# Optimization experiments

Measured on AMD Instinct MI355X. Metric: run time of the kernel, lower is better.

## Reference

```python
import jax, jax.numpy as jnp
import numpy as np

B, N, D = 2, 8192, 1024
H, Dh = 16, 64
P = H * Dh
EPS = 1e-6
DECAY_BIAS_SHIFT = 2.0


def setup_inputs() -> dict:
    key = jax.random.key(0)
    ks = jax.random.split(key, 7)
    s_in = 1.0 / np.sqrt(D)
    s_out = 1.0 / np.sqrt(P)
    return {
        "x": jax.random.normal(ks[0], (B, N, D), jnp.float32),
        "Wq": jax.random.normal(ks[1], (D, P), jnp.float32) * s_in,
        "Wk": jax.random.normal(ks[2], (D, P), jnp.float32) * s_in,
        "Wv": jax.random.normal(ks[3], (D, P), jnp.float32) * s_in,
        "Wo": jax.random.normal(ks[4], (P, D), jnp.float32) * s_out,
        "Wa": jax.random.normal(ks[5], (D, H), jnp.float32) * s_in,
        "ba": jnp.zeros((H,), jnp.float32),
    }


def _elu_plus_one(x):
    return jax.nn.elu(x) + 1.0


def _ssd_scan(q, k, v, a, eps):
    # q,k,v: (B,H,N,Dh); a: (B,H,N) in (0,1)
    # Recurrence: S_t = a_t*S_{t-1} + k_t v_t^T ; z_t = a_t*z_{t-1} + k_t
    # out_t = (q_t @ S_t) / (q_t . z_t + eps)
    qT = jnp.moveaxis(q, 2, 0)  # (N,B,H,Dh)
    kT = jnp.moveaxis(k, 2, 0)
    vT = jnp.moveaxis(v, 2, 0)
    aT = jnp.moveaxis(a, 2, 0)  # (N,B,H)

    Bb, Hh, _, Dk = q.shape
    Dv = v.shape[-1]
    S0 = jnp.zeros((Bb, Hh, Dk, Dv), q.dtype)
    z0 = jnp.zeros((Bb, Hh, Dk), q.dtype)

    def step(carry, inp):
        S, z = carry
        qt, kt, vt, at = inp
        S = at[..., None, None] * S + kt[..., :, None] * vt[..., None, :]
        z = at[..., None] * z + kt
        num = jnp.einsum("bhk,bhkv->bhv", qt, S)
        den = jnp.einsum("bhk,bhk->bh", qt, z) + eps
        return (S, z), num / den[..., None]

    _, outT = jax.lax.scan(step, (S0, z0), (qT, kT, vT, aT))
    return jnp.moveaxis(outT, 0, 2)  # (B,H,N,Dv)


def reference(x, Wq, Wk, Wv, Wo, Wa, ba):
    b, n, _ = x.shape
    q = (x @ Wq).reshape(b, n, H, Dh).transpose(0, 2, 1, 3)
    k = (x @ Wk).reshape(b, n, H, Dh).transpose(0, 2, 1, 3)
    v = (x @ Wv).reshape(b, n, H, Dh).transpose(0, 2, 1, 3)
    q = _elu_plus_one(q)
    k = _elu_plus_one(k)
    a = jax.nn.sigmoid(x @ Wa + ba + DECAY_BIAS_SHIFT)  # (B,N,H)
    a = a.transpose(0, 2, 1)  # (B,H,N)
    out = _ssd_scan(q, k, v, a, EPS)  # (B,H,N,Dh)
    out = out.transpose(0, 2, 1, 3).reshape(b, n, P)
    return out @ Wo
```

## Files before the change

kernel.cpp:

```cpp
#include <hip/hip_runtime.h>
#include <stdint.h>

#define HH 16
#define DH 64
#define DD 1024
#define PP 1024
#define NNLEN 8192
#define BBATCH 2
#define MM (BBATCH*NNLEN)
#define CCHUNK 128
#define LCH 64
#define NGRP 16
#define GCH 8
#define EPSV 1e-6f

typedef unsigned short u16;
typedef __attribute__((ext_vector_type(4))) unsigned short u16x4;
typedef __attribute__((ext_vector_type(8))) unsigned short u16x8;
typedef __attribute__((ext_vector_type(8))) __bf16 bf16x8;
typedef __attribute__((ext_vector_type(4))) float f32x4;

__device__ __forceinline__ u16 f2bf(float f) {
  unsigned x = __float_as_uint(f);
  return (u16)((x + 0x7fffu + ((x >> 16) & 1u)) >> 16);
}
__device__ __forceinline__ float bf2f(u16 u) {
  return __uint_as_float(((unsigned)u) << 16);
}

__device__ __forceinline__ void gl2lds16(const void* g, void* l) {
  __builtin_amdgcn_global_load_lds(
      reinterpret_cast<__attribute__((address_space(1))) void*>(
          reinterpret_cast<uintptr_t>(g)),
      reinterpret_cast<__attribute__((address_space(3))) void*>(
          reinterpret_cast<uintptr_t>(l)),
      16, 0, 0);
}

__device__ __forceinline__ bf16x8 ldsw(const u16* base, int row, int col) {
  union { u16x8 u; bf16x8 b; } cv;
  cv.u = *(const u16x8*)&base[row * 64 + (col ^ ((row & 7) << 3))];
  return cv.b;
}

__global__ __launch_bounds__(256)
void convert_x(const float* __restrict__ in, u16* __restrict__ out) {
  size_t i = ((size_t)blockIdx.x * 256 + threadIdx.x) * 8;
  f32x4 a = *(const f32x4*)(in + i);
  f32x4 b = *(const f32x4*)(in + i + 4);
  u16x8 o;
  o[0] = f2bf(a[0]); o[1] = f2bf(a[1]); o[2] = f2bf(a[2]); o[3] = f2bf(a[3]);
  o[4] = f2bf(b[0]); o[5] = f2bf(b[1]); o[6] = f2bf(b[2]); o[7] = f2bf(b[3]);
  *(u16x8*)(out + i) = o;
}

__global__ __launch_bounds__(256)
void wa_prep(const float* __restrict__ Wa, u16* __restrict__ WaT) {
  int idx = blockIdx.x * 256 + threadIdx.x;
  WaT[idx] = f2bf(Wa[(idx & 1023) * 16 + (idx >> 10)]);
}

__global__ __launch_bounds__(256)
void transpose_f32_bf16(const float* __restrict__ in, u16* __restrict__ out) {
  __shared__ float tile[32][33];
  int bx = blockIdx.x * 32, by = blockIdx.y * 32;
  int tx = threadIdx.x & 31, ty = threadIdx.x >> 5;
  for (int i = ty; i < 32; i += 8)
    tile[i][tx] = in[(size_t)(by + i) * 1024 + bx + tx];
  __syncthreads();
  for (int i = ty; i < 32; i += 8)
    out[(size_t)(bx + i) * 1024 + by + tx] = f2bf(tile[tx][i]);
}

__global__ __launch_bounds__(256)
void a_proj(const u16* __restrict__ xb, const u16* __restrict__ WaT,
            const float* __restrict__ ba, float* __restrict__ abuf) {
  __shared__ __align__(16) u16 As[256 * 32];
  __shared__ __align__(16) u16 Bs[16 * 32];
  const int tid = threadIdx.x;
  const int brow = blockIdx.x * 256;
  const int l = tid & 63, wid = tid >> 6;
  const int la = l & 15, kb8 = (l >> 4) * 8;
  const int sr = tid >> 2, se = (tid & 3) * 8;

  f32x4 acc[4];
#pragma unroll
  for (int mi = 0; mi < 4; ++mi) acc[mi] = (f32x4){0.f, 0.f, 0.f, 0.f};

  for (int kt = 0; kt < 32; ++kt) {
    const int k0 = kt * 32;
    __syncthreads();
#pragma unroll
    for (int i = 0; i < 4; ++i)
      gl2lds16(xb + (size_t)(brow + i * 64 + sr) * DD + k0 + se,
               &As[i * 2048 + wid * 512]);
    if (wid == 0)
      gl2lds16(WaT + (size_t)(l >> 2) * DD + k0 + (l & 3) * 8, &Bs[0]);
    __syncthreads();
    union { u16x8 u; bf16x8 b; } cvb;
    cvb.u = *(const u16x8*)&Bs[la * 32 + kb8];
#pragma unroll
    for (int mi = 0; mi < 4; ++mi) {
      union { u16x8 u; bf16x8 b; } cva;
      cva.u = *(const u16x8*)&As[(wid * 64 + mi * 16 + la) * 32 + kb8];
      acc[mi] = __builtin_amdgcn_mfma_f32_16x16x32_bf16(cva.b, cvb.b, acc[mi], 0, 0, 0);
    }
  }
  const float bav = ba[la];
#pragma unroll
  for (int mi = 0; mi < 4; ++mi)
#pragma unroll
    for (int rr = 0; rr < 4; ++rr) {
      int row = brow + wid * 64 + mi * 16 + ((l >> 4) << 2) + rr;
      float t = acc[mi][rr] + bav + 2.0f;
      abuf[(size_t)row * HH + la] = 1.f / (1.f + __expf(-t));
    }
}

template<int NCT, int ROUTE>
__global__ __launch_bounds__(512)
void gemm8p(const u16* __restrict__ A, const u16* __restrict__ Bt,
            void* __restrict__ Cout) {
  __shared__ __align__(16) u16 As[2][256 * 64];
  __shared__ __align__(16) u16 Bs[2][256 * 64];
  const int tid = threadIdx.x;
  const int nwg = gridDim.x;
  const int f = blockIdx.x;
  const int swz = (f & 7) * (nwg >> 3) + (f >> 3);
  const int brow = (swz / NCT) * 256;
  const int bcol = (swz % NCT) * 256;
  const int l = tid & 63;
  const int wid = tid >> 6;
  const int wr = wid >> 2;
  const int wc = wid & 3;
  const int la = l & 15, kb8 = (l >> 4) * 8;
  const int K = 1024;
  const int srow = l >> 3;
  const int scol = ((l & 7) * 8) ^ (srow << 3);
  const int ldso = (wid * 2) * 512;

  f32x4 acc[8][4];
#pragma unroll
  for (int i = 0; i < 8; ++i)
#pragma unroll
    for (int j = 0; j < 4; ++j) acc[i][j] = (f32x4){0.f, 0.f, 0.f, 0.f};

#pragma unroll
  for (int h = 0; h < 2; ++h)
#pragma unroll
    for (int j = 0; j < 2; ++j) {
      const int r0 = h * 128 + (wid * 2 + j) * 8 + srow;
      gl2lds16(A  + (size_t)(brow + r0) * K + scol, &As[0][h * 8192 + ldso + j * 512]);
      gl2lds16(Bt + (size_t)(bcol + r0) * K + scol, &Bs[0][h * 8192 + ldso + j * 512]);
    }
  asm volatile("s_waitcnt vmcnt(0)" ::: "memory");
  __builtin_amdgcn_s_barrier();

  const int NKT = K / 64;
  for (int kt = 0; kt < NKT; ++kt) {
    const u16* lA = As[kt & 1];
    const u16* lB = Bs[kt & 1];
    u16* nA = As[(kt + 1) & 1];
    u16* nB = Bs[(kt + 1) & 1];
    const int knext = (kt + 1) * 64;
    const bool more = (kt + 1 < NKT);

    bf16x8 af[4][2], bfr[2][2];
#pragma unroll
    for (int p = 0; p < 4; ++p) {
      const int miH = (p >> 1);
      const int niH = (p == 1 || p == 2) ? 1 : 0;
      const bool doA = (p == 0 || p == 2);
      const bool doB = (p != 2);
      if (doA) {
#pragma unroll
        for (int m2 = 0; m2 < 4; ++m2)
#pragma unroll
          for (int kk = 0; kk < 2; ++kk)
            af[m2][kk] = ldsw(lA, wr * 128 + miH * 64 + m2 * 16 + la, kk * 32 + kb8);
      }
      if (doB) {
#pragma unroll
        for (int n2 = 0; n2 < 2; ++n2)
#pragma unroll
          for (int kk = 0; kk < 2; ++kk)
            bfr[n2][kk] = ldsw(lB, wc * 64 + niH * 32 + n2 * 16 + la, kk * 32 + kb8);
      }
      if (more && p == 0) {
#pragma unroll
        for (int h = 0; h < 2; ++h)
#pragma unroll
          for (int j = 0; j < 2; ++j) {
            const int r0 = h * 128 + (wid * 2 + j) * 8 + srow;
            gl2lds16(A + (size_t)(brow + r0) * K + knext + scol,
                     nA + h * 8192 + ldso + j * 512);
          }
      }
      if (more && p == 1) {
#pragma unroll
        for (int h = 0; h < 2; ++h)
#pragma unroll
          for (int j = 0; j < 2; ++j) {
            const int r0 = h * 128 + (wid * 2 + j) * 8 + srow;
            gl2lds16(Bt + (size_t)(bcol + r0) * K + knext + scol,
                     nB + h * 8192 + ldso + j * 512);
          }
      }
      __builtin_amdgcn_s_barrier();
      __builtin_amdgcn_s_setprio(1);
#pragma unroll
      for (int m2 = 0; m2 < 4; ++m2)
#pragma unroll
        for (int n2 = 0; n2 < 2; ++n2)
#pragma unroll
          for (int kk = 0; kk < 2; ++kk)
            acc[miH * 4 + m2][niH * 2 + n2] = __builtin_amdgcn_mfma_f32_16x16x32_bf16(
                af[m2][kk], bfr[n2][kk], acc[miH * 4 + m2][niH * 2 + n2], 0, 0, 0);
      __builtin_amdgcn_s_setprio(0);
      if (p == 3) asm volatile("s_waitcnt vmcnt(0)" ::: "memory");
      __builtin_amdgcn_s_barrier();
    }
  }

  const int wrow = wr * 128, wcol = wc * 64;
  if (ROUTE) {
    u16* base = (u16*)Cout + (size_t)(bcol >> 10) * ((size_t)MM * 1024);
    const bool act = (bcol < 2048);
#pragma unroll
    for (int mi = 0; mi < 8; ++mi)
#pragma unroll
      for (int ni = 0; ni < 4; ++ni)
#pragma unroll
        for (int rr = 0; rr < 4; ++rr) {
          int row = brow + wrow + mi * 16 + ((l >> 4) << 2) + rr;
          int c2 = (bcol & 1023) + wcol + ni * 16 + la;
          float v = acc[mi][ni][rr];
          if (act) v = v > 0.f ? v + 1.f : __expf(v);
          base[(size_t)row * 1024 + c2] = f2bf(v);
        }
  } else {
#pragma unroll
    for (int mi = 0; mi < 8; ++mi)
#pragma unroll
      for (int ni = 0; ni < 4; ++ni)
#pragma unroll
        for (int rr = 0; rr < 4; ++rr) {
          int row = brow + wrow + mi * 16 + ((l >> 4) << 2) + rr;
          int col = bcol + wcol + ni * 16 + la;
          ((float*)Cout)[(size_t)row * 1024 + col] = acc[mi][ni][rr];
        }
  }
}

__global__ __launch_bounds__(256)
void chunk_local(const u16* __restrict__ kb, const u16* __restrict__ vb,
                 const float* __restrict__ abuf,
                 u16* __restrict__ Sbuf, float* __restrict__ zbuf,
                 float* __restrict__ cAbuf) {
  const int blk = blockIdx.x;
  const int c = blk & (CCHUNK - 1);
  const int h = (blk >> 7) & (HH - 1);
  const int b = blk >> 11;
  const int rowbase = b * NNLEN + c * LCH;
  __shared__ __align__(16) u16 KT[64 * 64];
  __shared__ __align__(16) u16 VTl[64 * 64];
  __shared__ float wsh[64];
  const int tid = threadIdx.x;
  const int r = tid >> 2, e = (tid & 3) * 16;

  const u16* kp = kb + (size_t)(rowbase + r) * PP + h * DH + e;
  const u16* vp = vb + (size_t)(rowbase + r) * PP + h * DH + e;
  u16x8 k0 = *(const u16x8*)kp, k1 = *(const u16x8*)(kp + 8);
  u16x8 v0 = *(const u16x8*)vp, v1 = *(const u16x8*)(vp + 8);

  if (tid < 64) {
    float v = __logf(abuf[(size_t)(rowbase + tid) * HH + h]);
#pragma unroll
    for (int d = 1; d < 64; d <<= 1) {
      float u = __shfl_up(v, d);
      if (tid >= d) v += u;
    }
    cAbuf[(size_t)blk * 64 + tid] = v;
    float tot = __shfl(v, 63);
    wsh[tid] = __expf(tot - v);
  }
  __syncthreads();

  {
    const float wt = wsh[r];
#pragma unroll
    for (int j = 0; j < 8; ++j) {
      int d0 = e + j, d1 = e + 8 + j;
      KT[d0 * 64 + (r ^ ((d0 & 7) << 3))] = f2bf(bf2f(k0[j]) * wt);
      KT[d1 * 64 + (r ^ ((d1 & 7) << 3))] = f2bf(bf2f(k1[j]) * wt);
      VTl[d0 * 64 + (r ^ ((d0 & 7) << 3))] = v0[j];
      VTl[d1 * 64 + (r ^ ((d1 & 7) << 3))] = v1[j];
    }
  }
  __syncthreads();

  const int l = tid & 63, w = tid >> 6;
  const int kb8 = (l >> 4) << 3, la = l & 15;
  f32x4 s[4];
#pragma unroll
  for (int ni = 0; ni < 4; ++ni) s[ni] = (f32x4){0.f, 0.f, 0.f, 0.f};
#pragma unroll
  for (int kk = 0; kk < 2; ++kk) {
    bf16x8 av = ldsw(VTl, 16 * w + la, kk * 32 + kb8);
#pragma unroll
    for (int ni = 0; ni < 4; ++ni)
      s[ni] = __builtin_amdgcn_mfma_f32_16x16x32_bf16(
          av, ldsw(KT, 16 * ni + la, kk * 32 + kb8), s[ni], 0, 0, 0);
  }
  u16* Sc = Sbuf + (size_t)blk * 4096;
  const int dw = 16 * w + ((l >> 4) << 2);
#pragma unroll
  for (int ni = 0; ni < 4; ++ni)
#pragma unroll
    for (int rr = 0; rr < 4; ++rr)
      Sc[(dw + rr) * 64 + 16 * ni + la] = f2bf(s[ni][rr]);

  {
    const int dk = tid >> 2, tq = (tid & 3) * 16, swk = (dk & 7) << 3;
    float zp = 0.f;
#pragma unroll
    for (int i = 0; i < 16; ++i) zp += bf2f(KT[dk * 64 + ((tq + i) ^ swk)]);
    zp += __shfl_xor(zp, 1);
    zp += __shfl_xor(zp, 2);
    if ((tid & 3) == 0) zbuf[(size_t)blk * 64 + dk] = zp;
  }
}

__global__ __launch_bounds__(256)
void scan_group(u16* __restrict__ Sbuf, float* __restrict__ zbuf,
                const float* __restrict__ cAbuf,
                float* __restrict__ GAgg, float* __restrict__ zGAgg,
                float* __restrict__ dpbuf) {
  const int j = blockIdx.x & 3;
  const int g = (blockIdx.x >> 2) & (NGRP - 1);
  const int bh = blockIdx.x >> 6;
  const int c0 = g * GCH;
  const size_t cb = (size_t)bh * CCHUNK;
  const int elem = j * 1024 + threadIdx.x * 4;

  float dch[GCH];
#pragma unroll
  for (int i = 0; i < GCH; ++i)
    dch[i] = __expf(cAbuf[(cb + c0 + i) * 64 + 63]);
  if (j == 0 && threadIdx.x == 0) {
    float rp = 1.f;
#pragma unroll
    for (int i = 0; i < GCH; ++i) { dpbuf[cb + c0 + i] = rp; rp *= dch[i]; }
  }

  f32x4 run = (f32x4){0.f, 0.f, 0.f, 0.f};
  u16x4 cur = *(const u16x4*)&Sbuf[(cb + c0) * 4096 + elem];
#pragma unroll
  for (int i = 0; i < GCH; ++i) {
    u16x4 nxt;
    if (i + 1 < GCH) nxt = *(const u16x4*)&Sbuf[(cb + c0 + i + 1) * 4096 + elem];
    u16x4 o;
#pragma unroll
    for (int jj = 0; jj < 4; ++jj) o[jj] = f2bf(run[jj]);
    *(u16x4*)&Sbuf[(cb + c0 + i) * 4096 + elem] = o;
#pragma unroll
    for (int jj = 0; jj < 4; ++jj) run[jj] = dch[i] * run[jj] + bf2f(cur[jj]);
    cur = nxt;
  }
  *(f32x4*)&GAgg[((size_t)bh * NGRP + g) * 4096 + elem] = run;

  if (j == 0 && threadIdx.x < 64) {
    const int t = threadIdx.x;
    float zr = 0.f;
#pragma unroll
    for (int i = 0; i < GCH; ++i) {
      float curz = zbuf[(cb + c0 + i) * 64 + t];
      zbuf[(cb + c0 + i) * 64 + t] = zr;
      zr = dch[i] * zr + curz;
    }
    zGAgg[((size_t)bh * NGRP + g) * 64 + t] = zr;
  }
}

__global__ __launch_bounds__(1024)
void scan_top(float* __restrict__ GAgg, float* __restrict__ zGAgg,
              const float* __restrict__ cAbuf) {
  const int bh = blockIdx.x;
  const size_t cb = (size_t)bh * CCHUNK;
  __shared__ float Dsh[NGRP];
  if (threadIdx.x < NGRP) {
    float s = 0.f;
#pragma unroll
    for (int i = 0; i < GCH; ++i)
      s += cAbuf[(cb + threadIdx.x * GCH + i) * 64 + 63];
    Dsh[threadIdx.x] = __expf(s);
  }
  __syncthreads();
  const int elem = threadIdx.x * 4;
  float* base = GAgg + (size_t)bh * NGRP * 4096;
  f32x4 run = (f32x4){0.f, 0.f, 0.f, 0.f};
  f32x4 cur = *(const f32x4*)&base[elem];
#pragma unroll
  for (int gg = 0; gg < NGRP; ++gg) {
    f32x4 nxt;
    if (gg + 1 < NGRP) nxt = *(const f32x4*)&base[(gg + 1) * 4096 + elem];
    *(f32x4*)&base[gg * 4096 + elem] = run;
    const float D = Dsh[gg];
#pragma unroll
    for (int jj = 0; jj < 4; ++jj) run[jj] = D * run[jj] + cur[jj];
    cur = nxt;
  }
  if (threadIdx.x < 64) {
    float* zb = zGAgg + (size_t)bh * NGRP * 64;
    float zr = 0.f;
#pragma unroll
    for (int gg = 0; gg < NGRP; ++gg) {
      float a = zb[gg * 64 + threadIdx.x];
      zb[gg * 64 + threadIdx.x] = zr;
      zr = Dsh[gg] * zr + a;
    }
  }
}

__global__ __launch_bounds__(256)
void chunk_out(u16* __restrict__ qb, const u16* __restrict__ kb,
               const u16* __restrict__ vb, const u16* __restrict__ Sbuf,
               const float* __restrict__ zbuf, const float* __restrict__ cAbuf,
               const float* __restrict__ GAgg, const float* __restrict__ zGAgg,
               const float* __restrict__ dpbuf) {
  const int blk = blockIdx.x;
  const int c = blk & (CCHUNK - 1);
  const int h = (blk >> 7) & (HH - 1);
  const int b = blk >> 11;
  const int bh = blk >> 7;
  const int g = c >> 3;
  const int rowbase = b * NNLEN + c * LCH;

  __shared__ __align__(16) u16 Qs[64 * 64];
  __shared__ __align__(16) u16 Ke[64 * 64];
  __shared__ __align__(16) u16 VT[64 * 64];
  __shared__ __align__(16) u16 STs[64 * 64];
  __shared__ __align__(16) u16 Pb[64 * 64];
  __shared__ float cAsh[64], zsh[64], denP[64], qzs[64];

  const int tid = threadIdx.x;
  const int r = tid >> 2, e = (tid & 3) * 16;
  const float dp = dpbuf[blk];

  const u16* qp = qb + (size_t)(rowbase + r) * PP + h * DH + e;
  const u16* kp = kb + (size_t)(rowbase + r) * PP + h * DH + e;
  const u16* vp = vb + (size_t)(rowbase + r) * PP + h * DH + e;
  u16x8 q0 = *(const u16x8*)qp, q1 = *(const u16x8*)(qp + 8);
  u16x8 k0 = *(const u16x8*)kp, k1 = *(const u16x8*)(kp + 8);
  u16x8 v0 = *(const u16x8*)vp, v1 = *(const u16x8*)(vp + 8);
  const u16* sp = Sbuf + (size_t)blk * 4096 + r * 64 + e;
  u16x8 p0 = *(const u16x8*)sp, p1 = *(const u16x8*)(sp + 8);
  const float* gp = GAgg + ((size_t)bh * NGRP + g) * 4096 + r * 64 + e;
  f32x4 g0 = *(const f32x4*)gp, g1 = *(const f32x4*)(gp + 4),
        g2 = *(const f32x4*)(gp + 8), g3 = *(const f32x4*)(gp + 12);
  if (tid < 64) {
    cAsh[tid] = cAbuf[(size_t)blk * 64 + tid];
    zsh[tid] = zbuf[(size_t)blk * 64 + tid]
             + dp * zGAgg[((size_t)bh * NGRP + g) * 64 + tid];
  }
  __syncthreads();

  {
    const float c0c = cAsh[31];
    const int sw = (r & 7) << 3;
    const float qsc = __expf(cAsh[r] - c0c);
    const float ksc = __expf(c0c - cAsh[r]);
    const float ssc = __expf(c0c);
    u16x8 t0, t1, u0, u1, w0, w1;
#pragma unroll
    for (int j = 0; j < 8; ++j) {
      t0[j] = f2bf(bf2f(q0[j]) * qsc);
      t1[j] = f2bf(bf2f(q1[j]) * qsc);
      u0[j] = f2bf(bf2f(k0[j]) * ksc);
      u1[j] = f2bf(bf2f(k1[j]) * ksc);
    }
#pragma unroll
    for (int j = 0; j < 4; ++j) {
      w0[j]     = f2bf((bf2f(p0[j])     + dp * g0[j]) * ssc);
      w0[4 + j] = f2bf((bf2f(p0[4 + j]) + dp * g1[j]) * ssc);
      w1[j]     = f2bf((bf2f(p1[j])     + dp * g2[j]) * ssc);
      w1[4 + j] = f2bf((bf2f(p1[4 + j]) + dp * g3[j]) * ssc);
    }
    *(u16x8*)&Qs[r * 64 + (e ^ sw)] = t0;
    *(u16x8*)&Qs[r * 64 + ((e + 8) ^ sw)] = t1;
    *(u16x8*)&Ke[r * 64 + (e ^ sw)] = u0;
    *(u16x8*)&Ke[r * 64 + ((e + 8) ^ sw)] = u1;
    *(u16x8*)&STs[r * 64 + (e ^ sw)] = w0;
    *(u16x8*)&STs[r * 64 + ((e + 8) ^ sw)] = w1;
#pragma unroll
    for (int j = 0; j < 8; ++j) {
      int d0 = e + j, d1 = e + 8 + j;
      VT[d0 * 64 + (r ^ ((d0 & 7) << 3))] = v0[j];
      VT[d1 * 64 + (r ^ ((d1 & 7) << 3))] = v1[j];
    }
    if (tid < 64) zsh[tid] *= ssc;
  }
  __syncthreads();

  const int l = tid & 63, w = tid >> 6;
  const int kb8 = (l >> 4) << 3, la = l & 15;

  bf16x8 aq[2];
  f32x4 p[4];
#pragma unroll
  for (int ni = 0; ni < 4; ++ni) p[ni] = (f32x4){0.f, 0.f, 0.f, 0.f};
#pragma unroll
  for (int kk = 0; kk < 2; ++kk) {
    aq[kk] = ldsw(Qs, 16 * w + la, kk * 32 + kb8);
#pragma unroll
    for (int ni = 0; ni < 4; ++ni)
      p[ni] = __builtin_amdgcn_mfma_f32_16x16x32_bf16(
          aq[kk], ldsw(Ke, 16 * ni + la, kk * 32 + kb8), p[ni], 0, 0, 0);
  }

  const int tw = 16 * w + ((l >> 4) << 2);
  float rsum[4] = {0.f, 0.f, 0.f, 0.f};
#pragma unroll
  for (int ni = 0; ni < 4; ++ni)
#pragma unroll
    for (int rr = 0; rr < 4; ++rr) {
      int s = 16 * ni + la, t = tw + rr;
      float v = (s <= t) ? p[ni][rr] : 0.f;
      p[ni][rr] = v;
      rsum[rr] += v;
    }
#pragma unroll
  for (int d = 1; d < 16; d <<= 1)
#pragma unroll
    for (int rr = 0; rr < 4; ++rr) rsum[rr] += __shfl_xor(rsum[rr], d);
  if (la == 0)
#pragma unroll
    for (int rr = 0; rr < 4; ++rr) denP[tw + rr] = rsum[rr];

#pragma unroll
  for (int ni = 0; ni < 4; ++ni)
#pragma unroll
    for (int rr = 0; rr < 4; ++rr) {
      int t = tw + rr, s = 16 * ni + la;
      Pb[t * 64 + (s ^ ((t & 7) << 3))] = f2bf(p[ni][rr]);
    }

  {
    const int tq = tid >> 2, dq = (tid & 3) * 16, swq = (tq & 7) << 3;
    float qzp = 0.f;
#pragma unroll
    for (int i = 0; i < 16; ++i)
      qzp += bf2f(Qs[tq * 64 + ((dq + i) ^ swq)]) * zsh[dq + i];
    qzp += __shfl_xor(qzp, 1);
    qzp += __shfl_xor(qzp, 2);
    if ((tid & 3) == 0) qzs[tq] = qzp;
  }
  __syncthreads();

  f32x4 o[4];
#pragma unroll
  for (int ni = 0; ni < 4; ++ni) o[ni] = (f32x4){0.f, 0.f, 0.f, 0.f};
#pragma unroll
  for (int kk = 0; kk < 2; ++kk) {
    bf16x8 ap = ldsw(Pb, 16 * w + la, kk * 32 + kb8);
#pragma unroll
    for (int ni = 0; ni < 4; ++ni)
      o[ni] = __builtin_amdgcn_mfma_f32_16x16x32_bf16(
          ap, ldsw(VT, 16 * ni + la, kk * 32 + kb8), o[ni], 0, 0, 0);
  }
#pragma unroll
  for (int kk = 0; kk < 2; ++kk)
#pragma unroll
    for (int ni = 0; ni < 4; ++ni)
      o[ni] = __builtin_amdgcn_mfma_f32_16x16x32_bf16(
          aq[kk], ldsw(STs, 16 * ni + la, kk * 32 + kb8), o[ni], 0, 0, 0);

  float dn[4];
#pragma unroll
  for (int rr = 0; rr < 4; ++rr) dn[rr] = qzs[tw + rr] + denP[tw + rr] + EPSV;
#pragma unroll
  for (int ni = 0; ni < 4; ++ni)
#pragma unroll
    for (int rr = 0; rr < 4; ++rr) {
      int t = tw + rr, dv = 16 * ni + la;
      qb[(size_t)(rowbase + t) * PP + h * DH + dv] = f2bf(o[ni][rr] / dn[rr]);
    }
}

extern "C" void kernel_launch(void* const* d_in, const int* in_sizes, int n_in,
                              void* d_out, int out_size, void* d_ws, size_t ws_size,
                              hipStream_t stream) {
  const float* x  = (const float*)d_in[0];
  const float* Wq = (const float*)d_in[1];
  const float* Wk = (const float*)d_in[2];
  const float* Wv = (const float*)d_in[3];
  const float* Wo = (const float*)d_in[4];
  const float* Wa = (const float*)d_in[5];
  const float* ba = (const float*)d_in[6];

  char* ws = (char*)d_ws;
  size_t off = 0;
  auto carve = [&](size_t bytes) {
    void* p = ws + off;
    off += (bytes + 255) & ~(size_t)255;
    return p;
  };
  u16* xb   = (u16*)carve((size_t)MM * DD * 2);
  u16* WqT  = (u16*)carve((size_t)PP * DD * 2);
  u16* WkT  = (u16*)carve((size_t)PP * DD * 2);
  u16* WvT  = (u16*)carve((size_t)PP * DD * 2);
  u16* WoT  = (u16*)carve((size_t)DD * PP * 2);
  u16* WaT  = (u16*)carve((size_t)HH * DD * 2);
  u16* qb   = (u16*)carve((size_t)MM * PP * 2);
  u16* kb   = (u16*)carve((size_t)MM * PP * 2);
  u16* vb   = (u16*)carve((size_t)MM * PP * 2);
  float* abuf  = (float*)carve((size_t)MM * HH * 4);
  u16*  Sbuf   = (u16*)carve((size_t)BBATCH * HH * CCHUNK * 4096 * 2);
  float* zbuf  = (float*)carve((size_t)BBATCH * HH * CCHUNK * 64 * 4);
  float* cAbuf = (float*)carve((size_t)BBATCH * HH * CCHUNK * 64 * 4);
  float* GAgg  = (float*)carve((size_t)BBATCH * HH * NGRP * 4096 * 4);
  float* zGAgg = (float*)carve((size_t)BBATCH * HH * NGRP * 64 * 4);
  float* dpbuf = (float*)carve((size_t)BBATCH * HH * CCHUNK * 4);

  transpose_f32_bf16<<<dim3(32, 32), 256, 0, stream>>>(Wq, WqT);
  transpose_f32_bf16<<<dim3(32, 32), 256, 0, stream>>>(Wk, WkT);
  transpose_f32_bf16<<<dim3(32, 32), 256, 0, stream>>>(Wv, WvT);
  transpose_f32_bf16<<<dim3(32, 32), 256, 0, stream>>>(Wo, WoT);
  wa_prep<<<64, 256, 0, stream>>>(Wa, WaT);
  convert_x<<<MM * DD / 8 / 256, 256, 0, stream>>>(x, xb);
  a_proj<<<MM / 256, 256, 0, stream>>>(xb, WaT, ba, abuf);

  gemm8p<12, 1><<<(MM / 256) * 12, 512, 0, stream>>>(xb, WqT, qb);

  chunk_local<<<BBATCH * HH * CCHUNK, 256, 0, stream>>>(kb, vb, abuf, Sbuf, zbuf, cAbuf);
  scan_group<<<BBATCH * HH * NGRP * 4, 256, 0, stream>>>(Sbuf, zbuf, cAbuf, GAgg, zGAgg, dpbuf);
  scan_top<<<BBATCH * HH, 1024, 0, stream>>>(GAgg, zGAgg, cAbuf);
  chunk_out<<<BBATCH * HH * CCHUNK, 256, 0, stream>>>(qb, kb, vb, Sbuf, zbuf, cAbuf,
                                                      GAgg, zGAgg, dpbuf);

  gemm8p<4, 0><<<(MM / 256) * 4, 512, 0, stream>>>(qb, WoT, (float*)d_out);
}
```

Before: 285.0 us.

## Fuse chunk-local state with group scan and simplify GEMM k-loop pipeline

Merges the chunk_local and scan_group kernels into one kernel, chunk_local_scan, where each block walks the 8 chunks of a group in sequence and carries the running state in registers. This avoids writing raw chunk states to Sbuf and then reading them back. The GEMM inner loop changes from four barrier-separated phases to two MFMA halves, with one combined prefetch and one barrier per k-step. Grid parallelism for the local state computation drops by a factor of 8, which risks lower occupancy. The GEMM now has less interleaving between loads and compute.

Result: faster. 272.5 us (-4.4%).

```diff
diff --git a/kernel.cpp b/kernel.cpp
--- a/kernel.cpp
+++ b/kernel.cpp
@@ -119,8 +119,8 @@
 
 template<int NCT, int ROUTE>
 __global__ __launch_bounds__(512)
-void gemm8p(const u16* __restrict__ A, const u16* __restrict__ Bt,
-            void* __restrict__ Cout) {
+void gemm_db(const u16* __restrict__ A, const u16* __restrict__ Bt,
+             void* __restrict__ Cout) {
   __shared__ __align__(16) u16 As[2][256 * 64];
   __shared__ __align__(16) u16 Bs[2][256 * 64];
   const int tid = threadIdx.x;
@@ -165,59 +165,61 @@
     const int knext = (kt + 1) * 64;
     const bool more = (kt + 1 < NKT);
 
-    bf16x8 af[4][2], bfr[2][2];
-#pragma unroll
-    for (int p = 0; p < 4; ++p) {
-      const int miH = (p >> 1);
-      const int niH = (p == 1 || p == 2) ? 1 : 0;
-      const bool doA = (p == 0 || p == 2);
-      const bool doB = (p != 2);
-      if (doA) {
-#pragma unroll
-        for (int m2 = 0; m2 < 4; ++m2)
-#pragma unroll
-          for (int kk = 0; kk < 2; ++kk)
-            af[m2][kk] = ldsw(lA, wr * 128 + miH * 64 + m2 * 16 + la, kk * 32 + kb8);
-      }
-      if (doB) {
-#pragma unroll
-        for (int n2 = 0; n2 < 2; ++n2)
-#pragma unroll
-          for (int kk = 0; kk < 2; ++kk)
-            bfr[n2][kk] = ldsw(lB, wc * 64 + niH * 32 + n2 * 16 + la, kk * 32 + kb8);
-      }
-      if (more && p == 0) {
-#pragma unroll
-        for (int h = 0; h < 2; ++h)
-#pragma unroll
-          for (int j = 0; j < 2; ++j) {
-            const int r0 = h * 128 + (wid * 2 + j) * 8 + srow;
-            gl2lds16(A + (size_t)(brow + r0) * K + knext + scol,
-                     nA + h * 8192 + ldso + j * 512);
-          }
-      }
-      if (more && p == 1) {
-#pragma unroll
-        for (int h = 0; h < 2; ++h)
-#pragma unroll
-          for (int j = 0; j < 2; ++j) {
-            const int r0 = h * 128 + (wid * 2 + j) * 8 + srow;
-            gl2lds16(Bt + (size_t)(bcol + r0) * K + knext + scol,
-                     nB + h * 8192 + ldso + j * 512);
-          }
-      }
-      __builtin_amdgcn_s_barrier();
-      __builtin_amdgcn_s_setprio(1);
-#pragma unroll
-      for (int m2 = 0; m2 < 4; ++m2)
-#pragma unroll
-        for (int n2 = 0; n2 < 2; ++n2)
-#pragma unroll
-          for (int kk = 0; kk < 2; ++kk)
-            acc[miH * 4 + m2][niH * 2 + n2] = __builtin_amdgcn_mfma_f32_16x16x32_bf16(
-                af[m2][kk], bfr[n2][kk], acc[miH * 4 + m2][niH * 2 + n2], 0, 0, 0);
-      __builtin_amdgcn_s_setprio(0);
-      if (p == 3) asm volatile("s_waitcnt vmcnt(0)" ::: "memory");
+    bf16x8 af[4][2], bfr[4][2];
+#pragma unroll
+    for (int m2 = 0; m2 < 4; ++m2)
+#pragma unroll
+      for (int kk = 0; kk < 2; ++kk)
+        af[m2][kk] = ldsw(lA, wr * 128 + m2 * 16 + la, kk * 32 + kb8);
+#pragma unroll
+    for (int n2 = 0; n2 < 4; ++n2)
+#pragma unroll
+      for (int kk = 0; kk < 2; ++kk)
+        bfr[n2][kk] = ldsw(lB, wc * 64 + n2 * 16 + la, kk * 32 + kb8);
+
+    __builtin_amdgcn_s_setprio(1);
+#pragma unroll
+    for (int m2 = 0; m2 < 4; ++m2)
+#pragma unroll
+      for (int n2 = 0; n2 < 4; ++n2)
+#pragma unroll
+        for (int kk = 0; kk < 2; ++kk)
+          acc[m2][n2] = __builtin_amdgcn_mfma_f32_16x16x32_bf16(
+              af[m2][kk], bfr[n2][kk], acc[m2][n2], 0, 0, 0);
+    __builtin_amdgcn_s_setprio(0);
+
+#pragma unroll
+    for (int m2 = 0; m2 < 4; ++m2)
+#pragma unroll
+      for (int kk = 0; kk < 2; ++kk)
+        af[m2][kk] = ldsw(lA, wr * 128 + 64 + m2 * 16 + la, kk * 32 + kb8);
+
+    if (more) {
+#pragma unroll
+      for (int h = 0; h < 2; ++h)
+#pragma unroll
+        for (int j = 0; j < 2; ++j) {
+          const int r0 = h * 128 + (wid * 2 + j) * 8 + srow;
+          gl2lds16(A  + (size_t)(brow + r0) * K + knext + scol,
+                   nA + h * 8192 + ldso + j * 512);
+          gl2lds16(Bt + (size_t)(bcol + r0) * K + knext + scol,
+                   nB + h * 8192 + ldso + j * 512);
+        }
+    }
+
+    __builtin_amdgcn_s_setprio(1);
+#pragma unroll
+    for (int m2 = 0; m2 < 4; ++m2)
+#pragma unroll
+      for (int n2 = 0; n2 < 4; ++n2)
+#pragma unroll
+        for (int kk = 0; kk < 2; ++kk)
+          acc[4 + m2][n2] = __builtin_amdgcn_mfma_f32_16x16x32_bf16(
+              af[m2][kk], bfr[n2][kk], acc[4 + m2][n2], 0, 0, 0);
+    __builtin_amdgcn_s_setprio(0);
+
+    if (more) {
+      asm volatile("s_waitcnt vmcnt(0)" ::: "memory");
       __builtin_amdgcn_s_barrier();
     }
   }
@@ -253,133 +255,118 @@
 }
 
 __global__ __launch_bounds__(256)
-void chunk_local(const u16* __restrict__ kb, const u16* __restrict__ vb,
-                 const float* __restrict__ abuf,
-                 u16* __restrict__ Sbuf, float* __restrict__ zbuf,
-                 float* __restrict__ cAbuf) {
-  const int blk = blockIdx.x;
-  const int c = blk & (CCHUNK - 1);
-  const int h = (blk >> 7) & (HH - 1);
-  const int b = blk >> 11;
-  const int rowbase = b * NNLEN + c * LCH;
+void chunk_local_scan(const u16* __restrict__ kb, const u16* __restrict__ vb,
+                      const float* __restrict__ abuf,
+                      u16* __restrict__ Sbuf, float* __restrict__ zbuf,
+                      float* __restrict__ cAbuf,
+                      float* __restrict__ GAgg, float* __restrict__ zGAgg,
+                      float* __restrict__ dpbuf) {
+  const int g = blockIdx.x & (NGRP - 1);
+  const int bh = blockIdx.x >> 4;
+  const int h = bh & (HH - 1);
+  const int b = bh >> 4;
   __shared__ __align__(16) u16 KT[64 * 64];
   __shared__ __align__(16) u16 VTl[64 * 64];
   __shared__ float wsh[64];
+  __shared__ float dchs;
   const int tid = threadIdx.x;
   const int r = tid >> 2, e = (tid & 3) * 16;
-
-  const u16* kp = kb + (size_t)(rowbase + r) * PP + h * DH + e;
-  const u16* vp = vb + (size_t)(rowbase + r) * PP + h * DH + e;
-  u16x8 k0 = *(const u16x8*)kp, k1 = *(const u16x8*)(kp + 8);
-  u16x8 v0 = *(const u16x8*)vp, v1 = *(const u16x8*)(vp + 8);
-
-  if (tid < 64) {
-    float v = __logf(abuf[(size_t)(rowbase + tid) * HH + h]);
-#pragma unroll
-    for (int d = 1; d < 64; d <<= 1) {
-      float u = __shfl_up(v, d);
-      if (tid >= d) v += u;
-    }
-    cAbuf[(size_t)blk * 64 + tid] = v;
-    float tot = __shfl(v, 63);
-    wsh[tid] = __expf(tot - v);
-  }
-  __syncthreads();
-
-  {
-    const float wt = wsh[r];
-#pragma unroll
-    for (int j = 0; j < 8; ++j) {
-      int d0 = e + j, d1 = e + 8 + j;
-      KT[d0 * 64 + (r ^ ((d0 & 7) << 3))] = f2bf(bf2f(k0[j]) * wt);
-      KT[d1 * 64 + (r ^ ((d1 & 7) << 3))] = f2bf(bf2f(k1[j]) * wt);
-      VTl[d0 * 64 + (r ^ ((d0 & 7) << 3))] = v0[j];
-      VTl[d1 * 64 + (r ^ ((d1 & 7) << 3))] = v1[j];
-    }
-  }
-  __syncthreads();
-
   const int l = tid & 63, w = tid >> 6;
   const int kb8 = (l >> 4) << 3, la = l & 15;
-  f32x4 s[4];
-#pragma unroll
-  for (int ni = 0; ni < 4; ++ni) s[ni] = (f32x4){0.f, 0.f, 0.f, 0.f};
-#pragma unroll
-  for (int kk = 0; kk < 2; ++kk) {
-    bf16x8 av = ldsw(VTl, 16 * w + la, kk * 32 + kb8);
+  const int dw = 16 * w + ((l >> 4) << 2);
+  const int dkz = tid >> 2, tqz = (tid & 3) * 16, swkz = (dkz & 7) << 3;
+
+  f32x4 run[4];
+#pragma unroll
+  for (int ni = 0; ni < 4; ++ni) run[ni] = (f32x4){0.f, 0.f, 0.f, 0.f};
+  float zrun = 0.f;
+  float rp = 1.f;
+
+  for (int i = 0; i < GCH; ++i) {
+    const int c = g * GCH + i;
+    const int blkc = bh * CCHUNK + c;
+    const int rowbase = b * NNLEN + c * LCH;
+
+    const u16* kp = kb + (size_t)(rowbase + r) * PP + h * DH + e;
+    const u16* vp = vb + (size_t)(rowbase + r) * PP + h * DH + e;
+    u16x8 k0 = *(const u16x8*)kp, k1 = *(const u16x8*)(kp + 8);
+    u16x8 v0 = *(const u16x8*)vp, v1 = *(const u16x8*)(vp + 8);
+
+    if (tid < 64) {
+      float v = __logf(abuf[(size_t)(rowbase + tid) * HH + h]);
+#pragma unroll
+      for (int d = 1; d < 64; d <<= 1) {
+        float u = __shfl_up(v, d);
+        if (tid >= d) v += u;
+      }
+      cAbuf[(size_t)blkc * 64 + tid] = v;
+      float tot = __shfl(v, 63);
+      wsh[tid] = __expf(tot - v);
+      if (tid == 0) dchs = __expf(tot);
+    }
+    __syncthreads();
+
+    {
+      const float wt = wsh[r];
+#pragma unroll
+      for (int j = 0; j < 8; ++j) {
+        int d0 = e + j, d1 = e + 8 + j;
+        KT[d0 * 64 + (r ^ ((d0 & 7) << 3))] = f2bf(bf2f(k0[j]) * wt);
+        KT[d1 * 64 + (r ^ ((d1 & 7) << 3))] = f2bf(bf2f(k1[j]) * wt);
+        VTl[d0 * 64 + (r ^ ((d0 & 7) << 3))] = v0[j];
+        VTl[d1 * 64 + (r ^ ((d1 & 7) << 3))] = v1[j];
+      }
+    }
+    __syncthreads();
+    const float dch = dchs;
+
+    f32x4 s[4];
+#pragma unroll
+    for (int ni = 0; ni < 4; ++ni) s[ni] = (f32x4){0.f, 0.f, 0.f, 0.f};
+#pragma unroll
+    for (int kk = 0; kk < 2; ++kk) {
+      bf16x8 av = ldsw(VTl, 16 * w + la, kk * 32 + kb8);
+#pragma unroll
+      for (int ni = 0; ni < 4; ++ni)
+        s[ni] = __builtin_amdgcn_mfma_f32_16x16x32_bf16(
+            av, ldsw(KT, 16 * ni + la, kk * 32 + kb8), s[ni], 0, 0, 0);
+    }
+
+    u16* Sc = Sbuf + (size_t)blkc * 4096;
 #pragma unroll
     for (int ni = 0; ni < 4; ++ni)
-      s[ni] = __builtin_amdgcn_mfma_f32_16x16x32_bf16(
-          av, ldsw(KT, 16 * ni + la, kk * 32 + kb8), s[ni], 0, 0, 0);
-  }
-  u16* Sc = Sbuf + (size_t)blk * 4096;
-  const int dw = 16 * w + ((l >> 4) << 2);
+#pragma unroll
+      for (int rr = 0; rr < 4; ++rr)
+        Sc[(dw + rr) * 64 + 16 * ni + la] = f2bf(run[ni][rr]);
+#pragma unroll
+    for (int ni = 0; ni < 4; ++ni)
+#pragma unroll
+      for (int rr = 0; rr < 4; ++rr)
+        run[ni][rr] = dch * run[ni][rr] + s[ni][rr];
+
+    {
+      float zp = 0.f;
+#pragma unroll
+      for (int i2 = 0; i2 < 16; ++i2)
+        zp += bf2f(KT[dkz * 64 + ((tqz + i2) ^ swkz)]);
+      zp += __shfl_xor(zp, 1);
+      zp += __shfl_xor(zp, 2);
+      if ((tid & 3) == 0) zbuf[(size_t)blkc * 64 + dkz] = zrun;
+      zrun = dch * zrun + zp;
+    }
+    if (tid == 0) dpbuf[blkc] = rp;
+    rp *= dch;
+    __syncthreads();
+  }
+
+  float* Ga = GAgg + ((size_t)bh * NGRP + g) * 4096;
 #pragma unroll
   for (int ni = 0; ni < 4; ++ni)
 #pragma unroll
     for (int rr = 0; rr < 4; ++rr)
-      Sc[(dw + rr) * 64 + 16 * ni + la] = f2bf(s[ni][rr]);
-
-  {
-    const int dk = tid >> 2, tq = (tid & 3) * 16, swk = (dk & 7) << 3;
-    float zp = 0.f;
-#pragma unroll
-    for (int i = 0; i < 16; ++i) zp += bf2f(KT[dk * 64 + ((tq + i) ^ swk)]);
-    zp += __shfl_xor(zp, 1);
-    zp += __shfl_xor(zp, 2);
-    if ((tid & 3) == 0) zbuf[(size_t)blk * 64 + dk] = zp;
-  }
-}
-
-__global__ __launch_bounds__(256)
-void scan_group(u16* __restrict__ Sbuf, float* __restrict__ zbuf,
-                const float* __restrict__ cAbuf,
-                float* __restrict__ GAgg, float* __restrict__ zGAgg,
-                float* __restrict__ dpbuf) {
-  const int j = blockIdx.x & 3;
-  const int g = (blockIdx.x >> 2) & (NGRP - 1);
-  const int bh = blockIdx.x >> 6;
-  const int c0 = g * GCH;
-  const size_t cb = (size_t)bh * CCHUNK;
-  const int elem = j * 1024 + threadIdx.x * 4;
-
-  float dch[GCH];
-#pragma unroll
-  for (int i = 0; i < GCH; ++i)
-    dch[i] = __expf(cAbuf[(cb + c0 + i) * 64 + 63]);
-  if (j == 0 && threadIdx.x == 0) {
-    float rp = 1.f;
-#pragma unroll
-    for (int i = 0; i < GCH; ++i) { dpbuf[cb + c0 + i] = rp; rp *= dch[i]; }
-  }
-
-  f32x4 run = (f32x4){0.f, 0.f, 0.f, 0.f};
-  u16x4 cur = *(const u16x4*)&Sbuf[(cb + c0) * 4096 + elem];
-#pragma unroll
-  for (int i = 0; i < GCH; ++i) {
-    u16x4 nxt;
-    if (i + 1 < GCH) nxt = *(const u16x4*)&Sbuf[(cb + c0 + i + 1) * 4096 + elem];
-    u16x4 o;
-#pragma unroll
-    for (int jj = 0; jj < 4; ++jj) o[jj] = f2bf(run[jj]);
-    *(u16x4*)&Sbuf[(cb + c0 + i) * 4096 + elem] = o;
-#pragma unroll
-    for (int jj = 0; jj < 4; ++jj) run[jj] = dch[i] * run[jj] + bf2f(cur[jj]);
-    cur = nxt;
-  }
-  *(f32x4*)&GAgg[((size_t)bh * NGRP + g) * 4096 + elem] = run;
-
-  if (j == 0 && threadIdx.x < 64) {
-    const int t = threadIdx.x;
-    float zr = 0.f;
-#pragma unroll
-    for (int i = 0; i < GCH; ++i) {
-      float curz = zbuf[(cb + c0 + i) * 64 + t];
-      zbuf[(cb + c0 + i) * 64 + t] = zr;
-      zr = dch[i] * zr + curz;
-    }
-    zGAgg[((size_t)bh * NGRP + g) * 64 + t] = zr;
-  }
+      Ga[(dw + rr) * 64 + 16 * ni + la] = run[ni][rr];
+  if ((tid & 3) == 0)
+    zGAgg[((size_t)bh * NGRP + g) * 64 + dkz] = zrun;
 }
 
 __global__ __launch_bounds__(1024)
@@ -630,13 +617,13 @@
   convert_x<<<MM * DD / 8 / 256, 256, 0, stream>>>(x, xb);
   a_proj<<<MM / 256, 256, 0, stream>>>(xb, WaT, ba, abuf);
 
-  gemm8p<12, 1><<<(MM / 256) * 12, 512, 0, stream>>>(xb, WqT, qb);
-
-  chunk_local<<<BBATCH * HH * CCHUNK, 256, 0, stream>>>(kb, vb, abuf, Sbuf, zbuf, cAbuf);
-  scan_group<<<BBATCH * HH * NGRP * 4, 256, 0, stream>>>(Sbuf, zbuf, cAbuf, GAgg, zGAgg, dpbuf);
+  gemm_db<12, 1><<<(MM / 256) * 12, 512, 0, stream>>>(xb, WqT, qb);
+
+  chunk_local_scan<<<BBATCH * HH * NGRP, 256, 0, stream>>>(
+      kb, vb, abuf, Sbuf, zbuf, cAbuf, GAgg, zGAgg, dpbuf);
   scan_top<<<BBATCH * HH, 1024, 0, stream>>>(GAgg, zGAgg, cAbuf);
   chunk_out<<<BBATCH * HH * CCHUNK, 256, 0, stream>>>(qb, kb, vb, Sbuf, zbuf, cAbuf,
                                                       GAgg, zGAgg, dpbuf);
 
-  gemm8p<4, 0><<<(MM / 256) * 4, 512, 0, stream>>>(qb, WoT, (float*)d_out);
-}
+  gemm_db<4, 0><<<(MM / 256) * 4, 512, 0, stream>>>(qb, WoT, (float*)d_out);
+}
```
